# Optimization experiments

Hardware: AMD Instinct MI355X
Metric: run time of the kernel (lower is better)

## Reference

```python
import jax, jax.numpy as jnp
import numpy as np

N = 100000   # nodes
E = 1600000  # edges
C = 128      # channels
EPS = 1e-5   # BatchNorm eps (PyG gnn.BatchNorm default)


def gcn_conv(x, W, b, src, dst, n):
    """PyG GCNConv: linear -> sym-normalized aggregation with self-loops -> bias."""
    h = x @ W                                      # [N, C]
    # degree with self-loops: in-degree at dst + 1
    deg = jnp.zeros((n,), h.dtype).at[dst].add(jnp.ones((), h.dtype)) + 1.0
    dinv = jax.lax.rsqrt(deg)                      # [N]
    norm = dinv[src] * dinv[dst]                   # [E]
    agg = jnp.zeros_like(h).at[dst].add(h[src] * norm[:, None])
    agg = agg + h * (dinv * dinv)[:, None]         # self-loop contribution
    return agg + b


def batch_norm(x, gamma, beta):
    """Training-mode BatchNorm over the node dimension (per-channel)."""
    mu = jnp.mean(x, axis=0)
    var = jnp.mean(jnp.square(x - mu), axis=0)     # biased variance
    return (x - mu) * jax.lax.rsqrt(var + EPS) * gamma + beta


def setup_inputs() -> dict:
    key = jax.random.key(0)
    ks = jax.random.split(key, 8)
    s = 1.0 / np.sqrt(C)
    x = jax.random.normal(ks[0], (N, C), dtype=jnp.float32)
    edge_index = jax.random.randint(ks[1], (2, E), 0, N, dtype=jnp.int64)
    W1 = jax.random.uniform(ks[2], (C, C), jnp.float32, -s, s)
    b1 = jax.random.uniform(ks[3], (C,), jnp.float32, -s, s)
    W2 = jax.random.uniform(ks[4], (C, C), jnp.float32, -s, s)
    b2 = jax.random.uniform(ks[5], (C,), jnp.float32, -s, s)
    gamma2 = jnp.ones((C,), jnp.float32)
    beta2 = jnp.zeros((C,), jnp.float32)
    return {"x": x, "W1": W1, "b1": b1, "W2": W2, "b2": b2,
            "gamma2": gamma2, "beta2": beta2, "edge_index": edge_index}


def reference(x, W1, b1, W2, b2, gamma2, beta2, edge_index):
    src, dst = edge_index[0], edge_index[1]
    identity = x
    # NOTE: original forward applies batch_norm2 after BOTH convs (batch_norm1 unused).
    h = jax.nn.relu(batch_norm(gcn_conv(x, W1, b1, src, dst, N), gamma2, beta2))
    h = batch_norm(gcn_conv(h, W2, b2, src, dst, N), gamma2, beta2)
    return jax.nn.relu(h + identity)
```

## Files before the change

kernel.cpp:

```cpp
#include <hip/hip_runtime.h>

#define N_NODES 100000
#define EDGES   1600000
#define CH      128
#define BN_EPS  1e-5f

#define BINS     782
#define CHUNKS   256
#define CHUNK_E  (EDGES / CHUNKS)
#define HM       (BINS * CHUNKS)
#define SCAN_NB  (HM / 256)
#define NREP     64

typedef __attribute__((ext_vector_type(8))) __bf16 bf16x8;
typedef __attribute__((ext_vector_type(4))) __bf16 bf16x4;
typedef __attribute__((ext_vector_type(2))) __bf16 bf16x2;
typedef __attribute__((ext_vector_type(4))) float  f32x4;

__global__ __launch_bounds__(256) void histo_kernel(const int* __restrict__ dst,
                                                    int* __restrict__ histo_g) {
    __shared__ int h[BINS];
    int t = threadIdx.x;
    for (int b = t; b < BINS; b += 256) h[b] = 0;
    __syncthreads();
    int base = blockIdx.x * CHUNK_E;
    for (int i = t; i < CHUNK_E; i += 256)
        atomicAdd(&h[dst[base + i] >> 7], 1);
    __syncthreads();
    for (int b = t; b < BINS; b += 256)
        histo_g[b * CHUNKS + blockIdx.x] = h[b];
}

__global__ __launch_bounds__(256) void scan1(const int* __restrict__ in,
                                             int* __restrict__ scanned,
                                             int* __restrict__ blocksum) {
    __shared__ int sh[2][256];
    int t = threadIdx.x;
    int i = blockIdx.x * 256 + t;
    int v = in[i];
    sh[0][t] = v;
    __syncthreads();
    int pp = 0;
    #pragma unroll
    for (int off = 1; off < 256; off <<= 1) {
        int val = sh[pp][t] + ((t >= off) ? sh[pp][t - off] : 0);
        sh[1 - pp][t] = val;
        pp = 1 - pp;
        __syncthreads();
    }
    int incl = sh[pp][t];
    scanned[i] = incl - v;
    if (t == 255) blocksum[blockIdx.x] = incl;
}

__global__ __launch_bounds__(1024) void scan2(int* __restrict__ blocksum) {
    __shared__ int sh[2][1024];
    int t = threadIdx.x;
    int v = (t < SCAN_NB) ? blocksum[t] : 0;
    sh[0][t] = v;
    __syncthreads();
    int pp = 0;
    #pragma unroll
    for (int off = 1; off < 1024; off <<= 1) {
        int val = sh[pp][t] + ((t >= off) ? sh[pp][t - off] : 0);
        sh[1 - pp][t] = val;
        pp = 1 - pp;
        __syncthreads();
    }
    if (t < SCAN_NB) blocksum[t] = sh[pp][t] - v;
}

__global__ __launch_bounds__(256) void scan3(int* __restrict__ scanned,
                                             const int* __restrict__ blocksum) {
    int i = blockIdx.x * 256 + threadIdx.x;
    scanned[i] += blocksum[blockIdx.x];
    if (i == HM - 1) scanned[HM] = EDGES;
}

__global__ __launch_bounds__(256) void place_kernel(const int* __restrict__ src,
                                                    const int* __restrict__ dst,
                                                    const int* __restrict__ scanned,
                                                    int* __restrict__ binned) {
    __shared__ int cur[BINS];
    int t = threadIdx.x;
    for (int b = t; b < BINS; b += 256)
        cur[b] = scanned[b * CHUNKS + blockIdx.x];
    __syncthreads();
    int base = blockIdx.x * CHUNK_E;
    for (int i = t; i < CHUNK_E; i += 256) {
        int d = dst[base + i];
        int s = src[base + i];
        int pos = atomicAdd(&cur[d >> 7], 1);
        binned[pos] = (s << 7) | (d & 127);
    }
}

__global__ __launch_bounds__(256) void bin_csr(const int* __restrict__ binned,
                                               const int* __restrict__ scanned,
                                               int* __restrict__ srcs,
                                               int* __restrict__ rowptr,
                                               float* __restrict__ dinv) {
    __shared__ int cnt[128];
    __shared__ int sc[2][128];
    __shared__ int base[128];
    __shared__ int cur[128];
    const int t = threadIdx.x;
    const int bin = blockIdx.x;
    if (t < 128) { cnt[t] = 0; cur[t] = 0; }
    __syncthreads();
    const int beg = scanned[bin * CHUNKS];
    const int end = scanned[bin * CHUNKS + CHUNKS];
    for (int e = beg + t; e < end; e += 256)
        atomicAdd(&cnt[binned[e] & 127], 1);
    __syncthreads();
    if (t < 128) sc[0][t] = cnt[t];
    __syncthreads();
    int pp = 0;
    #pragma unroll
    for (int off = 1; off < 128; off <<= 1) {
        if (t < 128) sc[1 - pp][t] = sc[pp][t] + ((t >= off) ? sc[pp][t - off] : 0);
        pp = 1 - pp;
        __syncthreads();
    }
    if (t < 128) {
        base[t] = beg + sc[pp][t] - cnt[t];
        int n = (bin << 7) + t;
        if (n < N_NODES) {
            rowptr[n] = base[t];
            dinv[n] = rsqrtf((float)cnt[t] + 1.0f);
        }
    }
    if (bin == 0 && t == 0) rowptr[N_NODES] = EDGES;
    __syncthreads();
    for (int e = beg + t; e < end; e += 256) {
        int p = binned[e];
        int dl = p & 127;
        int pos = base[dl] + atomicAdd(&cur[dl], 1);
        srcs[pos] = p >> 7;
    }
}

__global__ __launch_bounds__(256) void wtrans2(const float* __restrict__ W1,
                                               __bf16* __restrict__ Wt1,
                                               const float* __restrict__ W2,
                                               __bf16* __restrict__ Wt2) {
    int b = blockIdx.x;
    const float* W = (b < 64) ? W1 : W2;
    __bf16* Wt = (b < 64) ? Wt1 : Wt2;
    int idx = (b & 63) * 256 + threadIdx.x;
    int n = idx >> 7, k = idx & 127;
    Wt[idx] = (__bf16)W[k * 128 + n];
}

__global__ __launch_bounds__(256) void gemm_f32(const float* __restrict__ A,
                                                const __bf16* __restrict__ Wt,
                                                const float* __restrict__ dinv,
                                                __bf16* __restrict__ hs) {
    const int wave = threadIdx.x >> 6;
    const int rt = blockIdx.x * 4 + wave;
    if (rt >= N_NODES / 16) return;
    const int lane = threadIdx.x & 63;
    const int ln = lane & 15;
    const int quad = lane >> 4;
    const int arow = rt * 16 + ln;

    f32x4 acc[8];
    #pragma unroll
    for (int ct = 0; ct < 8; ++ct) acc[ct] = (f32x4){0.f, 0.f, 0.f, 0.f};

    #pragma unroll
    for (int k0 = 0; k0 < 128; k0 += 32) {
        const int k = k0 + quad * 8;
        float4 a0 = *(const float4*)(A + (size_t)arow * CH + k);
        float4 a1 = *(const float4*)(A + (size_t)arow * CH + k + 4);
        bf16x8 af;
        af[0] = (__bf16)a0.x; af[1] = (__bf16)a0.y;
        af[2] = (__bf16)a0.z; af[3] = (__bf16)a0.w;
        af[4] = (__bf16)a1.x; af[5] = (__bf16)a1.y;
        af[6] = (__bf16)a1.z; af[7] = (__bf16)a1.w;
        #pragma unroll
        for (int ct = 0; ct < 8; ++ct) {
            bf16x8 bfrag = *(const bf16x8*)(Wt + (size_t)(ct * 16 + ln) * CH + k);
            acc[ct] = __builtin_amdgcn_mfma_f32_16x16x32_bf16(af, bfrag, acc[ct], 0, 0, 0);
        }
    }

    #pragma unroll
    for (int r = 0; r < 4; ++r) {
        const int row_r = rt * 16 + quad * 4 + r;
        const float dr = dinv[row_r];
        __bf16* orow = hs + (size_t)row_r * CH + ln;
        #pragma unroll
        for (int ct = 0; ct < 8; ++ct)
            orow[ct * 16] = (__bf16)(acc[ct][r] * dr);
    }
}

__global__ __launch_bounds__(256) void gemm_bn(const __bf16* __restrict__ A,
                                               const __bf16* __restrict__ Wt,
                                               const float* __restrict__ dinv,
                                               const float* __restrict__ scale,
                                               const float* __restrict__ shift,
                                               __bf16* __restrict__ hs) {
    const int wave = threadIdx.x >> 6;
    const int rt = blockIdx.x * 4 + wave;
    if (rt >= N_NODES / 16) return;
    const int lane = threadIdx.x & 63;
    const int ln = lane & 15;
    const int quad = lane >> 4;
    const int arow = rt * 16 + ln;

    f32x4 acc[8];
    #pragma unroll
    for (int ct = 0; ct < 8; ++ct) acc[ct] = (f32x4){0.f, 0.f, 0.f, 0.f};

    #pragma unroll
    for (int k0 = 0; k0 < 128; k0 += 32) {
        const int k = k0 + quad * 8;
        bf16x8 av = *(const bf16x8*)(A + (size_t)arow * CH + k);
        bf16x8 af;
        #pragma unroll
        for (int j = 0; j < 8; ++j)
            af[j] = (__bf16)fmaxf(fmaf((float)av[j], scale[k + j], shift[k + j]), 0.f);
        #pragma unroll
        for (int ct = 0; ct < 8; ++ct) {
            bf16x8 bfrag = *(const bf16x8*)(Wt + (size_t)(ct * 16 + ln) * CH + k);
            acc[ct] = __builtin_amdgcn_mfma_f32_16x16x32_bf16(af, bfrag, acc[ct], 0, 0, 0);
        }
    }

    #pragma unroll
    for (int r = 0; r < 4; ++r) {
        const int row_r = rt * 16 + quad * 4 + r;
        const float dr = dinv[row_r];
        __bf16* orow = hs + (size_t)row_r * CH + ln;
        #pragma unroll
        for (int ct = 0; ct < 8; ++ct)
            orow[ct * 16] = (__bf16)(acc[ct][r] * dr);
    }
}

__global__ __launch_bounds__(256) void gather_agg(const __bf16* __restrict__ hs,
                                                  const int* __restrict__ srcs,
                                                  const int* __restrict__ rowptr,
                                                  const float* __restrict__ dinv,
                                                  __bf16* __restrict__ agg,
                                                  float* __restrict__ gpart) {
    __shared__ float red[4][64][4];
    const int wave = threadIdx.x >> 6;
    const int c2 = threadIdx.x & 63;
    const bf16x2* hp = (const bf16x2*)hs;

    float s0 = 0.f, ss0 = 0.f, s1 = 0.f, ss1 = 0.f;

    #pragma unroll
    for (int it = 0; it < 2; ++it) {
        const int n = __builtin_amdgcn_readfirstlane(blockIdx.x * 8 + wave * 2 + it);
        const int beg = rowptr[n];
        const int end = rowptr[n + 1];
        bf16x2 sv = hp[(size_t)n * 64 + c2];
        float ax = (float)sv[0], ay = (float)sv[1];
        int j = beg;
        for (; j + 8 <= end; j += 8) {
            int e0 = srcs[j + 0], e1 = srcs[j + 1], e2 = srcs[j + 2], e3 = srcs[j + 3];
            int e4 = srcs[j + 4], e5 = srcs[j + 5], e6 = srcs[j + 6], e7 = srcs[j + 7];
            bf16x2 v0 = hp[(size_t)e0 * 64 + c2];
            bf16x2 v1 = hp[(size_t)e1 * 64 + c2];
            bf16x2 v2 = hp[(size_t)e2 * 64 + c2];
            bf16x2 v3 = hp[(size_t)e3 * 64 + c2];
            bf16x2 v4 = hp[(size_t)e4 * 64 + c2];
            bf16x2 v5 = hp[(size_t)e5 * 64 + c2];
            bf16x2 v6 = hp[(size_t)e6 * 64 + c2];
            bf16x2 v7 = hp[(size_t)e7 * 64 + c2];
            ax += (((float)v0[0] + (float)v1[0]) + ((float)v2[0] + (float)v3[0]))
                + (((float)v4[0] + (float)v5[0]) + ((float)v6[0] + (float)v7[0]));
            ay += (((float)v0[1] + (float)v1[1]) + ((float)v2[1] + (float)v3[1]))
                + (((float)v4[1] + (float)v5[1]) + ((float)v6[1] + (float)v7[1]));
        }
        for (; j < end; ++j) {
            bf16x2 v = hp[(size_t)srcs[j] * 64 + c2];
            ax += (float)v[0];
            ay += (float)v[1];
        }
        float d = dinv[n];
        float ox = ax * d, oy = ay * d;
        bf16x2 o; o[0] = (__bf16)ox; o[1] = (__bf16)oy;
        ((bf16x2*)agg)[(size_t)n * 64 + c2] = o;
        s0 += ox; ss0 += ox * ox;
        s1 += oy; ss1 += oy * oy;
    }

    f32x4 rv; rv[0] = s0; rv[1] = ss0; rv[2] = s1; rv[3] = ss1;
    *(f32x4*)red[wave][c2] = rv;
    __syncthreads();
    const int t = threadIdx.x;
    float v = red[0][t >> 2][t & 3] + red[1][t >> 2][t & 3] +
              red[2][t >> 2][t & 3] + red[3][t >> 2][t & 3];
    atomicAdd(&gpart[(blockIdx.x & (NREP - 1)) * 256 + t], v);
}

__global__ void bn_final(const float* __restrict__ gpart,
                         const float* __restrict__ gamma,
                         const float* __restrict__ beta,
                         float* __restrict__ scale,
                         float* __restrict__ shift) {
    int c = threadIdx.x;
    int c2 = c >> 1, odd = c & 1;
    float s = 0.f, ss = 0.f;
    for (int r = 0; r < NREP; ++r) {
        s  += gpart[r * 256 + c2 * 4 + 2 * odd];
        ss += gpart[r * 256 + c2 * 4 + 2 * odd + 1];
    }
    const float invN = 1.0f / (float)N_NODES;
    float mu = s * invN;
    float var = ss * invN - mu * mu;
    float sc = gamma[c] * rsqrtf(var + BN_EPS);
    scale[c] = sc;
    shift[c] = beta[c] - mu * sc;
}

__global__ __launch_bounds__(256) void bn_apply_res_relu(const __bf16* __restrict__ v,
                                                         const float* __restrict__ scale,
                                                         const float* __restrict__ shift,
                                                         const float* __restrict__ xin,
                                                         float* __restrict__ outv) {
    int i = blockIdx.x * 256 + threadIdx.x;
    int cg = i & 31;
    bf16x4 a4 = ((const bf16x4*)v)[i];
    float4 r = ((const float4*)xin)[i];
    float4 sc = ((const float4*)scale)[cg];
    float4 sh = ((const float4*)shift)[cg];
    float4 a;
    a.x = fmaxf(fmaf((float)a4[0], sc.x, sh.x) + r.x, 0.f);
    a.y = fmaxf(fmaf((float)a4[1], sc.y, sh.y) + r.y, 0.f);
    a.z = fmaxf(fmaf((float)a4[2], sc.z, sh.z) + r.z, 0.f);
    a.w = fmaxf(fmaf((float)a4[3], sc.w, sh.w) + r.w, 0.f);
    ((float4*)outv)[i] = a;
}

extern "C" void kernel_launch(void* const* d_in, const int* in_sizes, int n_in,
                              void* d_out, int out_size, void* d_ws, size_t ws_size,
                              hipStream_t stream) {
    const float* x      = (const float*)d_in[0];
    const float* W1     = (const float*)d_in[1];
    const float* W2     = (const float*)d_in[3];
    const float* gamma2 = (const float*)d_in[5];
    const float* beta2  = (const float*)d_in[6];
    const int*   ei     = (const int*)d_in[7];
    const int*   srcI   = ei;
    const int*   dstI   = ei + EDGES;
    float* out = (float*)d_out;

    char* ws = (char*)d_ws;
    __bf16* agg      = (__bf16*)(ws);
    __bf16* hs       = (__bf16*)(ws + 25600000);
    int*    binned   = (int*)   (ws + 51200000);
    int*    srcs     = (int*)   (ws + 57600000);
    int*    histo_g  = (int*)   (ws + 64000000);
    int*    scanned  = (int*)   (ws + 64801024);
    int*    blocksum = (int*)   (ws + 65602048);
    float*  dinv     = (float*) (ws + 65605632);
    int*    rowptr   = (int*)   (ws + 66005632);
    __bf16* Wt1      = (__bf16*)(ws + 66405888);
    __bf16* Wt2      = (__bf16*)(ws + 66438656);
    float*  gpart    = (float*) (ws + 66471424);
    float*  scale1   = (float*) (ws + 66536960);
    float*  shift1   = scale1 + 128;
    float*  scale2   = scale1 + 256;
    float*  shift2   = scale1 + 384;

    const int ELEM4_BLOCKS  = (N_NODES * 32) / 256;
    const int GEMM_BLOCKS   = (N_NODES / 16 + 3) / 4;
    const int GATHER_BLOCKS = N_NODES / 8;

    histo_kernel<<<CHUNKS, 256, 0, stream>>>(dstI, histo_g);
    scan1<<<SCAN_NB, 256, 0, stream>>>(histo_g, scanned, blocksum);
    scan2<<<1, 1024, 0, stream>>>(blocksum);
    scan3<<<SCAN_NB, 256, 0, stream>>>(scanned, blocksum);
    place_kernel<<<CHUNKS, 256, 0, stream>>>(srcI, dstI, scanned, binned);
    bin_csr<<<BINS, 256, 0, stream>>>(binned, scanned, srcs, rowptr, dinv);
    wtrans2<<<128, 256, 0, stream>>>(W1, Wt1, W2, Wt2);

    gemm_f32<<<GEMM_BLOCKS, 256, 0, stream>>>(x, Wt1, dinv, hs);
    hipMemsetAsync(gpart, 0, NREP * 256 * sizeof(float), stream);
    gather_agg<<<GATHER_BLOCKS, 256, 0, stream>>>(hs, srcs, rowptr, dinv, agg, gpart);
    bn_final<<<1, 128, 0, stream>>>(gpart, gamma2, beta2, scale1, shift1);

    gemm_bn<<<GEMM_BLOCKS, 256, 0, stream>>>(agg, Wt2, dinv, scale1, shift1, hs);
    hipMemsetAsync(gpart, 0, NREP * 256 * sizeof(float), stream);
    gather_agg<<<GATHER_BLOCKS, 256, 0, stream>>>(hs, srcs, rowptr, dinv, agg, gpart);
    bn_final<<<1, 128, 0, stream>>>(gpart, gamma2, beta2, scale2, shift2);
    bn_apply_res_relu<<<ELEM4_BLOCKS, 256, 0, stream>>>(agg, scale2, shift2, x, out);
}
```

Measured before the change: 382.8 us.

## Store node features in channel-chunked layout and gather per chunk

Result: slower. 433.7 us (+13.3%).

```diff
diff --git a/kernel.cpp b/kernel.cpp
--- a/kernel.cpp
+++ b/kernel.cpp
@@ -11,6 +11,9 @@
 #define HM       (BINS * CHUNKS)
 #define SCAN_NB  (HM / 256)
 #define NREP     64
+
+#define GCHUNKS  8
+#define GBLKS    (N_NODES / 32)
 
 typedef __attribute__((ext_vector_type(8))) __bf16 bf16x8;
 typedef __attribute__((ext_vector_type(4))) __bf16 bf16x4;
@@ -143,8 +146,10 @@
 __global__ __launch_bounds__(256) void wtrans2(const float* __restrict__ W1,
                                                __bf16* __restrict__ Wt1,
                                                const float* __restrict__ W2,
-                                               __bf16* __restrict__ Wt2) {
+                                               __bf16* __restrict__ Wt2,
+                                               unsigned* __restrict__ hspad) {
     int b = blockIdx.x;
+    if (b == 0 && threadIdx.x < 16) hspad[threadIdx.x] = 0u;
     const float* W = (b < 64) ? W1 : W2;
     __bf16* Wt = (b < 64) ? Wt1 : Wt2;
     int idx = (b & 63) * 256 + threadIdx.x;
@@ -189,10 +194,9 @@
     for (int r = 0; r < 4; ++r) {
         const int row_r = rt * 16 + quad * 4 + r;
         const float dr = dinv[row_r];
-        __bf16* orow = hs + (size_t)row_r * CH + ln;
         #pragma unroll
         for (int ct = 0; ct < 8; ++ct)
-            orow[ct * 16] = (__bf16)(acc[ct][r] * dr);
+            hs[((size_t)ct * N_NODES + row_r) * 16 + ln] = (__bf16)(acc[ct][r] * dr);
     }
 }
 
@@ -217,7 +221,7 @@
     #pragma unroll
     for (int k0 = 0; k0 < 128; k0 += 32) {
         const int k = k0 + quad * 8;
-        bf16x8 av = *(const bf16x8*)(A + (size_t)arow * CH + k);
+        bf16x8 av = *(const bf16x8*)(A + ((size_t)(k >> 4) * N_NODES + arow) * 16 + (k & 15));
         bf16x8 af;
         #pragma unroll
         for (int j = 0; j < 8; ++j)
@@ -233,70 +237,79 @@
     for (int r = 0; r < 4; ++r) {
         const int row_r = rt * 16 + quad * 4 + r;
         const float dr = dinv[row_r];
-        __bf16* orow = hs + (size_t)row_r * CH + ln;
         #pragma unroll
         for (int ct = 0; ct < 8; ++ct)
-            orow[ct * 16] = (__bf16)(acc[ct][r] * dr);
-    }
-}
-
-__global__ __launch_bounds__(256) void gather_agg(const __bf16* __restrict__ hs,
-                                                  const int* __restrict__ srcs,
-                                                  const int* __restrict__ rowptr,
-                                                  const float* __restrict__ dinv,
-                                                  __bf16* __restrict__ agg,
-                                                  float* __restrict__ gpart) {
-    __shared__ float red[4][64][4];
+            hs[((size_t)ct * N_NODES + row_r) * 16 + ln] = (__bf16)(acc[ct][r] * dr);
+    }
+}
+
+__global__ __launch_bounds__(256) void gather_chunk(const __bf16* __restrict__ hs2,
+                                                    const int* __restrict__ srcs,
+                                                    const int* __restrict__ rowptr,
+                                                    const float* __restrict__ dinv,
+                                                    __bf16* __restrict__ agg2,
+                                                    float* __restrict__ gpart) {
+    __shared__ float red[4][8][8][4];
     const int wave = threadIdx.x >> 6;
-    const int c2 = threadIdx.x & 63;
-    const bf16x2* hp = (const bf16x2*)hs;
-
-    float s0 = 0.f, ss0 = 0.f, s1 = 0.f, ss1 = 0.f;
-
-    #pragma unroll
-    for (int it = 0; it < 2; ++it) {
-        const int n = __builtin_amdgcn_readfirstlane(blockIdx.x * 8 + wave * 2 + it);
-        const int beg = rowptr[n];
-        const int end = rowptr[n + 1];
-        bf16x2 sv = hp[(size_t)n * 64 + c2];
-        float ax = (float)sv[0], ay = (float)sv[1];
-        int j = beg;
-        for (; j + 8 <= end; j += 8) {
-            int e0 = srcs[j + 0], e1 = srcs[j + 1], e2 = srcs[j + 2], e3 = srcs[j + 3];
-            int e4 = srcs[j + 4], e5 = srcs[j + 5], e6 = srcs[j + 6], e7 = srcs[j + 7];
-            bf16x2 v0 = hp[(size_t)e0 * 64 + c2];
-            bf16x2 v1 = hp[(size_t)e1 * 64 + c2];
-            bf16x2 v2 = hp[(size_t)e2 * 64 + c2];
-            bf16x2 v3 = hp[(size_t)e3 * 64 + c2];
-            bf16x2 v4 = hp[(size_t)e4 * 64 + c2];
-            bf16x2 v5 = hp[(size_t)e5 * 64 + c2];
-            bf16x2 v6 = hp[(size_t)e6 * 64 + c2];
-            bf16x2 v7 = hp[(size_t)e7 * 64 + c2];
-            ax += (((float)v0[0] + (float)v1[0]) + ((float)v2[0] + (float)v3[0]))
-                + (((float)v4[0] + (float)v5[0]) + ((float)v6[0] + (float)v7[0]));
-            ay += (((float)v0[1] + (float)v1[1]) + ((float)v2[1] + (float)v3[1]))
-                + (((float)v4[1] + (float)v5[1]) + ((float)v6[1] + (float)v7[1]));
+    const int lane = threadIdx.x & 63;
+    const int g  = lane >> 3;
+    const int cp = lane & 7;
+    const int chunk = blockIdx.x / GBLKS;
+    const int nb = blockIdx.x - chunk * GBLKS;
+    const unsigned* hp = (const unsigned*)hs2 + (size_t)chunk * (N_NODES * 8);
+    const int zidx = (GCHUNKS - chunk) * N_NODES;
+
+    const int n = nb * 32 + wave * 8 + g;
+    const int beg = rowptr[n];
+    const int end = rowptr[n + 1];
+    int dm = end - beg;
+    dm = max(dm, __shfl_xor(dm, 8));
+    dm = max(dm, __shfl_xor(dm, 16));
+    dm = max(dm, __shfl_xor(dm, 32));
+    dm = __builtin_amdgcn_readfirstlane(dm);
+
+    bf16x2 s2 = __builtin_bit_cast(bf16x2, hp[(n << 3) + cp]);
+    float ax = (float)s2[0], ay = (float)s2[1];
+
+    for (int t0 = 0; t0 < dm; t0 += 8) {
+        int e[8];
+        #pragma unroll
+        for (int u = 0; u < 8; ++u) {
+            int jt = beg + t0 + u;
+            int sval = srcs[min(jt, EDGES - 1)];
+            e[u] = (jt < end) ? sval : zidx;
         }
-        for (; j < end; ++j) {
-            bf16x2 v = hp[(size_t)srcs[j] * 64 + c2];
-            ax += (float)v[0];
-            ay += (float)v[1];
+        unsigned v[8];
+        #pragma unroll
+        for (int u = 0; u < 8; ++u)
+            v[u] = hp[(e[u] << 3) + cp];
+        #pragma unroll
+        for (int u = 0; u < 8; ++u) {
+            bf16x2 b = __builtin_bit_cast(bf16x2, v[u]);
+            ax += (float)b[0];
+            ay += (float)b[1];
         }
-        float d = dinv[n];
-        float ox = ax * d, oy = ay * d;
-        bf16x2 o; o[0] = (__bf16)ox; o[1] = (__bf16)oy;
-        ((bf16x2*)agg)[(size_t)n * 64 + c2] = o;
-        s0 += ox; ss0 += ox * ox;
-        s1 += oy; ss1 += oy * oy;
-    }
-
-    f32x4 rv; rv[0] = s0; rv[1] = ss0; rv[2] = s1; rv[3] = ss1;
-    *(f32x4*)red[wave][c2] = rv;
+    }
+
+    const float d = dinv[n];
+    const float ox = ax * d, oy = ay * d;
+    bf16x2 o; o[0] = (__bf16)ox; o[1] = (__bf16)oy;
+    ((bf16x2*)agg2 + (size_t)chunk * (N_NODES * 8))[(n << 3) + cp] = o;
+
+    f32x4 rv; rv[0] = ox; rv[1] = ox * ox; rv[2] = oy; rv[3] = oy * oy;
+    *(f32x4*)red[wave][g][cp] = rv;
     __syncthreads();
     const int t = threadIdx.x;
-    float v = red[0][t >> 2][t & 3] + red[1][t >> 2][t & 3] +
-              red[2][t >> 2][t & 3] + red[3][t >> 2][t & 3];
-    atomicAdd(&gpart[(blockIdx.x & (NREP - 1)) * 256 + t], v);
+    if (t < 32) {
+        const int tcp = t >> 2, comp = t & 3;
+        float acc = 0.f;
+        #pragma unroll
+        for (int w = 0; w < 4; ++w)
+            #pragma unroll
+            for (int gg = 0; gg < 8; ++gg)
+                acc += red[w][gg][tcp][comp];
+        atomicAdd(&gpart[(blockIdx.x & (NREP - 1)) * 256 + (chunk * 8 + tcp) * 4 + comp], acc);
+    }
 }
 
 __global__ void bn_final(const float* __restrict__ gpart,
@@ -325,8 +338,8 @@
                                                          const float* __restrict__ xin,
                                                          float* __restrict__ outv) {
     int i = blockIdx.x * 256 + threadIdx.x;
-    int cg = i & 31;
-    bf16x4 a4 = ((const bf16x4*)v)[i];
+    int n = i >> 5, cg = i & 31;
+    bf16x4 a4 = *(const bf16x4*)(v + ((size_t)(cg >> 2) * N_NODES + n) * 16 + (cg & 3) * 4);
     float4 r = ((const float4*)xin)[i];
     float4 sc = ((const float4*)scale)[cg];
     float4 sh = ((const float4*)shift)[cg];
@@ -352,26 +365,27 @@
     float* out = (float*)d_out;
 
     char* ws = (char*)d_ws;
-    __bf16* agg      = (__bf16*)(ws);
-    __bf16* hs       = (__bf16*)(ws + 25600000);
-    int*    binned   = (int*)   (ws + 51200000);
-    int*    srcs     = (int*)   (ws + 57600000);
-    int*    histo_g  = (int*)   (ws + 64000000);
-    int*    scanned  = (int*)   (ws + 64801024);
-    int*    blocksum = (int*)   (ws + 65602048);
-    float*  dinv     = (float*) (ws + 65605632);
-    int*    rowptr   = (int*)   (ws + 66005632);
-    __bf16* Wt1      = (__bf16*)(ws + 66405888);
-    __bf16* Wt2      = (__bf16*)(ws + 66438656);
-    float*  gpart    = (float*) (ws + 66471424);
-    float*  scale1   = (float*) (ws + 66536960);
-    float*  shift1   = scale1 + 128;
-    float*  scale2   = scale1 + 256;
-    float*  shift2   = scale1 + 384;
+    __bf16*   agg      = (__bf16*)(ws);
+    __bf16*   hs       = (__bf16*)(ws + 25600000);
+    unsigned* hspad    = (unsigned*)(ws + 51200000);
+    int*      binned   = (int*)   (ws + 51200128);
+    int*      srcs     = (int*)   (ws + 57600128);
+    int*      histo_g  = (int*)   (ws + 64000128);
+    int*      scanned  = (int*)   (ws + 64800896);
+    int*      blocksum = (int*)   (ws + 65601680);
+    float*    dinv     = (float*) (ws + 65604864);
+    int*      rowptr   = (int*)   (ws + 66004864);
+    __bf16*   Wt1      = (__bf16*)(ws + 66404928);
+    __bf16*   Wt2      = (__bf16*)(ws + 66437696);
+    float*    gpart    = (float*) (ws + 66470464);
+    float*    scale1   = (float*) (ws + 66536000);
+    float*    shift1   = scale1 + 128;
+    float*    scale2   = scale1 + 256;
+    float*    shift2   = scale1 + 384;
 
     const int ELEM4_BLOCKS  = (N_NODES * 32) / 256;
     const int GEMM_BLOCKS   = (N_NODES / 16 + 3) / 4;
-    const int GATHER_BLOCKS = N_NODES / 8;
+    const int GATHER_BLOCKS = GCHUNKS * GBLKS;
 
     histo_kernel<<<CHUNKS, 256, 0, stream>>>(dstI, histo_g);
     scan1<<<SCAN_NB, 256, 0, stream>>>(histo_g, scanned, blocksum);
@@ -379,16 +393,16 @@
     scan3<<<SCAN_NB, 256, 0, stream>>>(scanned, blocksum);
     place_kernel<<<CHUNKS, 256, 0, stream>>>(srcI, dstI, scanned, binned);
     bin_csr<<<BINS, 256, 0, stream>>>(binned, scanned, srcs, rowptr, dinv);
-    wtrans2<<<128, 256, 0, stream>>>(W1, Wt1, W2, Wt2);
+    wtrans2<<<128, 256, 0, stream>>>(W1, Wt1, W2, Wt2, hspad);
 
     gemm_f32<<<GEMM_BLOCKS, 256, 0, stream>>>(x, Wt1, dinv, hs);
     hipMemsetAsync(gpart, 0, NREP * 256 * sizeof(float), stream);
-    gather_agg<<<GATHER_BLOCKS, 256, 0, stream>>>(hs, srcs, rowptr, dinv, agg, gpart);
+    gather_chunk<<<GATHER_BLOCKS, 256, 0, stream>>>(hs, srcs, rowptr, dinv, agg, gpart);
     bn_final<<<1, 128, 0, stream>>>(gpart, gamma2, beta2, scale1, shift1);
 
     gemm_bn<<<GEMM_BLOCKS, 256, 0, stream>>>(agg, Wt2, dinv, scale1, shift1, hs);
     hipMemsetAsync(gpart, 0, NREP * 256 * sizeof(float), stream);
-    gather_agg<<<GATHER_BLOCKS, 256, 0, stream>>>(hs, srcs, rowptr, dinv, agg, gpart);
+    gather_chunk<<<GATHER_BLOCKS, 256, 0, stream>>>(hs, srcs, rowptr, dinv, agg, gpart);
     bn_final<<<1, 128, 0, stream>>>(gpart, gamma2, beta2, scale2, shift2);
     bn_apply_res_relu<<<ELEM4_BLOCKS, 256, 0, stream>>>(agg, scale2, shift2, x, out);
 }
```

## Fold scan3 into consumers and interleave two-node gathers with padded zero row

Applied to the files above, without the earlier changes.

After: 379.5 us (median of 2 runs). Within noise of the previous version (-0.9%).

```diff
diff --git a/kernel.cpp b/kernel.cpp
--- a/kernel.cpp
+++ b/kernel.cpp
@@ -70,21 +70,15 @@
     if (t < SCAN_NB) blocksum[t] = sh[pp][t] - v;
 }
 
-__global__ __launch_bounds__(256) void scan3(int* __restrict__ scanned,
-                                             const int* __restrict__ blocksum) {
-    int i = blockIdx.x * 256 + threadIdx.x;
-    scanned[i] += blocksum[blockIdx.x];
-    if (i == HM - 1) scanned[HM] = EDGES;
-}
-
 __global__ __launch_bounds__(256) void place_kernel(const int* __restrict__ src,
                                                     const int* __restrict__ dst,
                                                     const int* __restrict__ scanned,
+                                                    const int* __restrict__ blocksum,
                                                     int* __restrict__ binned) {
     __shared__ int cur[BINS];
     int t = threadIdx.x;
     for (int b = t; b < BINS; b += 256)
-        cur[b] = scanned[b * CHUNKS + blockIdx.x];
+        cur[b] = scanned[b * CHUNKS + blockIdx.x] + blocksum[b];
     __syncthreads();
     int base = blockIdx.x * CHUNK_E;
     for (int i = t; i < CHUNK_E; i += 256) {
@@ -97,6 +91,7 @@
 
 __global__ __launch_bounds__(256) void bin_csr(const int* __restrict__ binned,
                                                const int* __restrict__ scanned,
+                                               const int* __restrict__ blocksum,
                                                int* __restrict__ srcs,
                                                int* __restrict__ rowptr,
                                                float* __restrict__ dinv) {
@@ -108,8 +103,9 @@
     const int bin = blockIdx.x;
     if (t < 128) { cnt[t] = 0; cur[t] = 0; }
     __syncthreads();
-    const int beg = scanned[bin * CHUNKS];
-    const int end = scanned[bin * CHUNKS + CHUNKS];
+    const int beg = scanned[bin * CHUNKS] + blocksum[bin];
+    const int end = (bin == BINS - 1) ? EDGES
+                    : (scanned[(bin + 1) * CHUNKS] + blocksum[bin + 1]);
     for (int e = beg + t; e < end; e += 256)
         atomicAdd(&cnt[binned[e] & 127], 1);
     __syncthreads();
@@ -143,8 +139,10 @@
 __global__ __launch_bounds__(256) void wtrans2(const float* __restrict__ W1,
                                                __bf16* __restrict__ Wt1,
                                                const float* __restrict__ W2,
-                                               __bf16* __restrict__ Wt2) {
+                                               __bf16* __restrict__ Wt2,
+                                               unsigned* __restrict__ hspad) {
     int b = blockIdx.x;
+    if (b == 0 && threadIdx.x < 64) hspad[threadIdx.x] = 0u;
     const float* W = (b < 64) ? W1 : W2;
     __bf16* Wt = (b < 64) ? Wt1 : Wt2;
     int idx = (b & 63) * 256 + threadIdx.x;
@@ -251,46 +249,57 @@
     const int c2 = threadIdx.x & 63;
     const bf16x2* hp = (const bf16x2*)hs;
 
-    float s0 = 0.f, ss0 = 0.f, s1 = 0.f, ss1 = 0.f;
-
-    #pragma unroll
-    for (int it = 0; it < 2; ++it) {
-        const int n = __builtin_amdgcn_readfirstlane(blockIdx.x * 8 + wave * 2 + it);
-        const int beg = rowptr[n];
-        const int end = rowptr[n + 1];
-        bf16x2 sv = hp[(size_t)n * 64 + c2];
-        float ax = (float)sv[0], ay = (float)sv[1];
-        int j = beg;
-        for (; j + 8 <= end; j += 8) {
-            int e0 = srcs[j + 0], e1 = srcs[j + 1], e2 = srcs[j + 2], e3 = srcs[j + 3];
-            int e4 = srcs[j + 4], e5 = srcs[j + 5], e6 = srcs[j + 6], e7 = srcs[j + 7];
-            bf16x2 v0 = hp[(size_t)e0 * 64 + c2];
-            bf16x2 v1 = hp[(size_t)e1 * 64 + c2];
-            bf16x2 v2 = hp[(size_t)e2 * 64 + c2];
-            bf16x2 v3 = hp[(size_t)e3 * 64 + c2];
-            bf16x2 v4 = hp[(size_t)e4 * 64 + c2];
-            bf16x2 v5 = hp[(size_t)e5 * 64 + c2];
-            bf16x2 v6 = hp[(size_t)e6 * 64 + c2];
-            bf16x2 v7 = hp[(size_t)e7 * 64 + c2];
-            ax += (((float)v0[0] + (float)v1[0]) + ((float)v2[0] + (float)v3[0]))
-                + (((float)v4[0] + (float)v5[0]) + ((float)v6[0] + (float)v7[0]));
-            ay += (((float)v0[1] + (float)v1[1]) + ((float)v2[1] + (float)v3[1]))
-                + (((float)v4[1] + (float)v5[1]) + ((float)v6[1] + (float)v7[1]));
+    const int n0 = __builtin_amdgcn_readfirstlane(blockIdx.x * 8 + wave * 2);
+    const int n1 = n0 + 1;
+    const int b0 = rowptr[n0];
+    const int e0 = rowptr[n0 + 1];
+    const int e1 = rowptr[n1 + 1];
+    const int b1 = e0;
+    const int d0 = e0 - b0, d1 = e1 - b1;
+    const int nt = (max(d0, d1) + 7) >> 3;
+
+    bf16x2 sv0 = hp[(size_t)n0 * 64 + c2];
+    bf16x2 sv1 = hp[(size_t)n1 * 64 + c2];
+    float ax0 = (float)sv0[0], ay0 = (float)sv0[1];
+    float ax1 = (float)sv1[0], ay1 = (float)sv1[1];
+
+    int j0 = b0, j1 = b1;
+    for (int t = 0; t < nt; ++t) {
+        int ea[8], eb[8];
+        #pragma unroll
+        for (int u = 0; u < 8; ++u) {
+            int sa = srcs[j0 + u];
+            int sb = srcs[j1 + u];
+            ea[u] = (j0 + u < e0) ? sa : N_NODES;
+            eb[u] = (j1 + u < e1) ? sb : N_NODES;
         }
-        for (; j < end; ++j) {
-            bf16x2 v = hp[(size_t)srcs[j] * 64 + c2];
-            ax += (float)v[0];
-            ay += (float)v[1];
-        }
-        float d = dinv[n];
-        float ox = ax * d, oy = ay * d;
-        bf16x2 o; o[0] = (__bf16)ox; o[1] = (__bf16)oy;
-        ((bf16x2*)agg)[(size_t)n * 64 + c2] = o;
-        s0 += ox; ss0 += ox * ox;
-        s1 += oy; ss1 += oy * oy;
-    }
-
-    f32x4 rv; rv[0] = s0; rv[1] = ss0; rv[2] = s1; rv[3] = ss1;
+        bf16x2 va[8], vb[8];
+        #pragma unroll
+        for (int u = 0; u < 8; ++u) va[u] = hp[(size_t)ea[u] * 64 + c2];
+        #pragma unroll
+        for (int u = 0; u < 8; ++u) vb[u] = hp[(size_t)eb[u] * 64 + c2];
+        ax0 += (((float)va[0][0] + (float)va[1][0]) + ((float)va[2][0] + (float)va[3][0]))
+             + (((float)va[4][0] + (float)va[5][0]) + ((float)va[6][0] + (float)va[7][0]));
+        ay0 += (((float)va[0][1] + (float)va[1][1]) + ((float)va[2][1] + (float)va[3][1]))
+             + (((float)va[4][1] + (float)va[5][1]) + ((float)va[6][1] + (float)va[7][1]));
+        ax1 += (((float)vb[0][0] + (float)vb[1][0]) + ((float)vb[2][0] + (float)vb[3][0]))
+             + (((float)vb[4][0] + (float)vb[5][0]) + ((float)vb[6][0] + (float)vb[7][0]));
+        ay1 += (((float)vb[0][1] + (float)vb[1][1]) + ((float)vb[2][1] + (float)vb[3][1]))
+             + (((float)vb[4][1] + (float)vb[5][1]) + ((float)vb[6][1] + (float)vb[7][1]));
+        j0 += 8; j1 += 8;
+    }
+
+    const float dd0 = dinv[n0], dd1 = dinv[n1];
+    const float o0x = ax0 * dd0, o0y = ay0 * dd0;
+    const float o1x = ax1 * dd1, o1y = ay1 * dd1;
+    bf16x2 o0; o0[0] = (__bf16)o0x; o0[1] = (__bf16)o0y;
+    bf16x2 o1; o1[0] = (__bf16)o1x; o1[1] = (__bf16)o1y;
+    ((bf16x2*)agg)[(size_t)n0 * 64 + c2] = o0;
+    ((bf16x2*)agg)[(size_t)n1 * 64 + c2] = o1;
+
+    f32x4 rv;
+    rv[0] = o0x + o1x; rv[1] = o0x * o0x + o1x * o1x;
+    rv[2] = o0y + o1y; rv[3] = o0y * o0y + o1y * o1y;
     *(f32x4*)red[wave][c2] = rv;
     __syncthreads();
     const int t = threadIdx.x;
@@ -352,22 +361,23 @@
     float* out = (float*)d_out;
 
     char* ws = (char*)d_ws;
-    __bf16* agg      = (__bf16*)(ws);
-    __bf16* hs       = (__bf16*)(ws + 25600000);
-    int*    binned   = (int*)   (ws + 51200000);
-    int*    srcs     = (int*)   (ws + 57600000);
-    int*    histo_g  = (int*)   (ws + 64000000);
-    int*    scanned  = (int*)   (ws + 64801024);
-    int*    blocksum = (int*)   (ws + 65602048);
-    float*  dinv     = (float*) (ws + 65605632);
-    int*    rowptr   = (int*)   (ws + 66005632);
-    __bf16* Wt1      = (__bf16*)(ws + 66405888);
-    __bf16* Wt2      = (__bf16*)(ws + 66438656);
-    float*  gpart    = (float*) (ws + 66471424);
-    float*  scale1   = (float*) (ws + 66536960);
-    float*  shift1   = scale1 + 128;
-    float*  scale2   = scale1 + 256;
-    float*  shift2   = scale1 + 384;
+    __bf16*   agg      = (__bf16*)(ws);
+    __bf16*   hs       = (__bf16*)(ws + 25600000);
+    unsigned* hspad    = (unsigned*)(ws + 51200000);
+    int*      binned   = (int*)   (ws + 51200256);
+    int*      srcs     = (int*)   (ws + 57600256);
+    int*      histo_g  = (int*)   (ws + 64000256);
+    int*      scanned  = (int*)   (ws + 64801024);
+    int*      blocksum = (int*)   (ws + 65601792);
+    float*    dinv     = (float*) (ws + 65604920);
+    int*      rowptr   = (int*)   (ws + 66004920);
+    __bf16*   Wt1      = (__bf16*)(ws + 66404928);
+    __bf16*   Wt2      = (__bf16*)(ws + 66437696);
+    float*    gpart    = (float*) (ws + 66470464);
+    float*    scale1   = (float*) (ws + 66536000);
+    float*    shift1   = scale1 + 128;
+    float*    scale2   = scale1 + 256;
+    float*    shift2   = scale1 + 384;
 
     const int ELEM4_BLOCKS  = (N_NODES * 32) / 256;
     const int GEMM_BLOCKS   = (N_NODES / 16 + 3) / 4;
@@ -376,10 +386,9 @@
     histo_kernel<<<CHUNKS, 256, 0, stream>>>(dstI, histo_g);
     scan1<<<SCAN_NB, 256, 0, stream>>>(histo_g, scanned, blocksum);
     scan2<<<1, 1024, 0, stream>>>(blocksum);
-    scan3<<<SCAN_NB, 256, 0, stream>>>(scanned, blocksum);
-    place_kernel<<<CHUNKS, 256, 0, stream>>>(srcI, dstI, scanned, binned);
-    bin_csr<<<BINS, 256, 0, stream>>>(binned, scanned, srcs, rowptr, dinv);
-    wtrans2<<<128, 256, 0, stream>>>(W1, Wt1, W2, Wt2);
+    place_kernel<<<CHUNKS, 256, 0, stream>>>(srcI, dstI, scanned, blocksum, binned);
+    bin_csr<<<BINS, 256, 0, stream>>>(binned, scanned, blocksum, srcs, rowptr, dinv);
+    wtrans2<<<128, 256, 0, stream>>>(W1, Wt1, W2, Wt2, hspad);
 
     gemm_f32<<<GEMM_BLOCKS, 256, 0, stream>>>(x, Wt1, dinv, hs);
     hipMemsetAsync(gpart, 0, NREP * 256 * sizeof(float), stream);
```
